# Performance work log

Hardware: AMD Instinct MI355X
Metric: run time of the kernel (lower is better)

The kernel has to match this reference:

```python
import jax, jax.numpy as jnp
import numpy as np

EPS = 1e-5
NUM_HEADS = 16

def layernorm(x, g, b):
    mu = jnp.mean(x, axis=-1, keepdims=True)
    var = jnp.mean(jnp.square(x - mu), axis=-1, keepdims=True)
    return (x - mu) * jax.lax.rsqrt(var + EPS) * g + b

def setup_inputs() -> dict:
    key = jax.random.key(0)
    ks = jax.random.split(key, 5)
    B, N, C = 2, 2048, 1024
    s_in = 1.0 / np.sqrt(C)
    return {
        "x": jax.random.normal(ks[0], (B, N, C), jnp.float32),
        "ln1_g": jnp.ones((C,), jnp.float32),
        "ln1_b": jnp.zeros((C,), jnp.float32),
        "w_qk": jax.random.normal(ks[1], (C, 2 * C), jnp.float32) * s_in,
        "w_v": jax.random.normal(ks[2], (C, C), jnp.float32) * s_in,
        "ln2_g": jnp.ones((C,), jnp.float32),
        "ln2_b": jnp.zeros((C,), jnp.float32),
        "w_proj": jax.random.normal(ks[3], (C, C), jnp.float32) * s_in,
        "b_proj": jnp.zeros((C,), jnp.float32),
    }

def reference(x, ln1_g, ln1_b, w_qk, w_v, ln2_g, ln2_b, w_proj, b_proj):
    B, N, C = x.shape
    H = NUM_HEADS
    hd = C // H
    scale = hd ** (-0.5)
    xn = layernorm(x, ln1_g, ln1_b)
    # qk: [B,N,2C] -> q,k each [B,H,N,hd]
    qk = (xn @ w_qk).reshape(B, N, 2, H, hd).transpose(2, 0, 3, 1, 4)
    q, k = qk[0], qk[1]
    v = (xn @ w_v).reshape(B, N, H, hd).transpose(0, 2, 1, 3)  # [B,H,N,hd]
    attn = jnp.einsum("bhqd,bhkd->bhqk", q, k) * scale
    attn = jax.nn.softmax(attn, axis=-1)
    out = jnp.einsum("bhqk,bhkd->bhqd", attn, v)  # [B,H,N,hd]
    out = out.transpose(0, 2, 1, 3).reshape(B, N, C)
    out = layernorm(out, ln2_g, ln2_b)
    return out @ w_proj + b_proj
```

## Files before the change

kernel.cpp:

```cpp
#include <hip/hip_runtime.h>
#include <hip/hip_bf16.h>


typedef __attribute__((ext_vector_type(8))) short short8;
typedef __attribute__((ext_vector_type(4))) short short4v;
typedef __attribute__((ext_vector_type(4))) float float4v;

__device__ __forceinline__ unsigned short f2bf(float f) {
    unsigned u = __builtin_bit_cast(unsigned, f);
    return (unsigned short)((u + 0x7FFFu + ((u >> 16) & 1u)) >> 16);
}
__device__ __forceinline__ unsigned packbf2(float lo, float hi) {
    return __builtin_amdgcn_perm(__builtin_bit_cast(unsigned, hi) + 0x8000u,
                                 __builtin_bit_cast(unsigned, lo) + 0x8000u,
                                 0x07060302u);
}
__device__ __forceinline__ void gll16(const unsigned short* g, unsigned short* l) {
    __builtin_amdgcn_global_load_lds(
        (const __attribute__((address_space(1))) unsigned int*)g,
        (__attribute__((address_space(3))) unsigned int*)l, 16, 0, 0);
}

__global__ __launch_bounds__(256) void prep(
    const float* __restrict__ x, const float* __restrict__ g1, const float* __restrict__ b1,
    const float* __restrict__ w_qk, const float* __restrict__ w_v,
    const float* __restrict__ w_proj, const float* __restrict__ g2,
    const float* __restrict__ b2,
    unsigned short* __restrict__ xn, unsigned short* __restrict__ wqkvT,
    unsigned short* __restrict__ wgT, float* __restrict__ u, float* __restrict__ w0) {
    __shared__ float sh[32 * 33];
    const int bid = blockIdx.x, tid = threadIdx.x;
    if (bid < 4096) {
        const float4 v = reinterpret_cast<const float4*>(x + (size_t)bid * 1024)[tid];
        float s  = v.x + v.y + v.z + v.w;
        float sq = v.x * v.x + v.y * v.y + v.z * v.z + v.w * v.w;
#pragma unroll
        for (int off = 32; off >= 1; off >>= 1) {
            s  += __shfl_xor(s, off, 64);
            sq += __shfl_xor(sq, off, 64);
        }
        const int w = tid >> 6, lane = tid & 63;
        if (lane == 0) { sh[w] = s; sh[4 + w] = sq; }
        __syncthreads();
        s  = sh[0] + sh[1] + sh[2] + sh[3];
        sq = sh[4] + sh[5] + sh[6] + sh[7];
        const float mu = s * (1.f / 1024.f);
        const float rstd = rsqrtf(sq * (1.f / 1024.f) - mu * mu + 1e-5f);
        const float4 gv = reinterpret_cast<const float4*>(g1)[tid];
        const float4 bv = reinterpret_cast<const float4*>(b1)[tid];
        ushort4 o;
        o.x = f2bf((v.x - mu) * rstd * gv.x + bv.x);
        o.y = f2bf((v.y - mu) * rstd * gv.y + bv.y);
        o.z = f2bf((v.z - mu) * rstd * gv.z + bv.z);
        o.w = f2bf((v.w - mu) * rstd * gv.w + bv.w);
        *reinterpret_cast<ushort4*>(&xn[(size_t)bid * 1024 + tid * 4]) = o;
    } else {
        const float* in; unsigned short* out; int Cc, bx, by; bool doU = false;
        if (bid < 6144)      { int t = bid - 4096; in = w_qk;   out = wqkvT;               Cc = 2048; bx = t & 63; by = t >> 6; }
        else if (bid < 7168) { int t = bid - 6144; in = w_v;    out = wqkvT + 2048 * 1024; Cc = 1024; bx = t & 31; by = t >> 5; }
        else                 { int t = bid - 7168; in = w_proj; out = wgT; doU = true;     Cc = 1024; bx = t & 31; by = t >> 5; }
        const int c0 = bx * 32, r0 = by * 32;
        const int tx = tid & 31, ty = tid >> 5;
#pragma unroll
        for (int i = 0; i < 32; i += 8)
            sh[(ty + i) * 33 + tx] = in[(size_t)(r0 + ty + i) * Cc + c0 + tx];
        __syncthreads();
        const float scale = doU ? g2[r0 + tx] : 1.f;
        const float b2v   = doU ? b2[r0 + tx] : 0.f;
#pragma unroll
        for (int i = 0; i < 32; i += 8) {
            const float raw = sh[tx * 33 + ty + i];
            const float sc  = raw * scale;
            out[(size_t)(c0 + ty + i) * 1024 + r0 + tx] = f2bf(sc);
            if (doU) {
                float pu = sc, pw = raw * b2v;
#pragma unroll
                for (int off = 1; off <= 16; off <<= 1) {
                    pu += __shfl_xor(pu, off, 64);
                    pw += __shfl_xor(pw, off, 64);
                }
                if (tx == 0) {
                    atomicAdd(&u[c0 + ty + i], pu);
                    atomicAdd(&w0[c0 + ty + i], pw);
                }
            }
        }
    }
}

__device__ __forceinline__ void stage_tiles(const unsigned short* __restrict__ A,
                                            const unsigned short* __restrict__ Bt,
                                            int K, int m0, int n0, int k0,
                                            unsigned short* As, unsigned short* Bs,
                                            int w, int ls, int sg) {
#pragma unroll
    for (int i = 0; i < 4; i++) {
        const int r = w * 32 + i * 8 + ls;
        const int g = (sg ^ ls) * 8;
        gll16(&A[(size_t)(m0 + r) * K + k0 + g], &As[(w * 32 + i * 8) * 64]);
        gll16(&Bt[(size_t)(n0 + r) * K + k0 + g], &Bs[(w * 32 + i * 8) * 64]);
    }
}

__device__ __forceinline__ void gemm128_core(const unsigned short* __restrict__ A,
                                             const unsigned short* __restrict__ Bt,
                                             int K, int m0, int n0,
                                             unsigned short* As, unsigned short* Bs,
                                             float4v acc[4][4]) {
    const int tid = threadIdx.x, lane = tid & 63, w = tid >> 6;
    const int wr = (w >> 1) * 64, wc = (w & 1) * 64;
    const int quad = lane >> 4, l16 = lane & 15;
    const int ls = lane >> 3, sg = lane & 7;
#pragma unroll
    for (int mi = 0; mi < 4; mi++)
#pragma unroll
        for (int ni = 0; ni < 4; ni++) acc[mi][ni] = float4v{0.f, 0.f, 0.f, 0.f};

    const int NS = K >> 6;
    stage_tiles(A, Bt, K, m0, n0, 0, As, Bs, w, ls, sg);
    for (int s = 0; s < NS; s++) {
        __syncthreads();
        const int cur = (s & 1) << 13;
        if (s + 1 < NS)
            stage_tiles(A, Bt, K, m0, n0, (s + 1) << 6,
                        As + (((s + 1) & 1) << 13), Bs + (((s + 1) & 1) << 13),
                        w, ls, sg);
        const unsigned short* Ac = As + cur;
        const unsigned short* Bc = Bs + cur;
#pragma unroll
        for (int ks = 0; ks < 2; ks++) {
            short8 af[4], bfr[4];
#pragma unroll
            for (int mi = 0; mi < 4; mi++) {
                const int r = wr + mi * 16 + l16;
                af[mi] = *reinterpret_cast<const short8*>(
                    &Ac[r * 64 + ((ks * 4 + quad) ^ (r & 7)) * 8]);
            }
#pragma unroll
            for (int ni = 0; ni < 4; ni++) {
                const int r = wc + ni * 16 + l16;
                bfr[ni] = *reinterpret_cast<const short8*>(
                    &Bc[r * 64 + ((ks * 4 + quad) ^ (r & 7)) * 8]);
            }
#pragma unroll
            for (int mi = 0; mi < 4; mi++)
#pragma unroll
                for (int ni = 0; ni < 4; ni++)
                    acc[mi][ni] = __builtin_amdgcn_mfma_f32_16x16x32_bf16(
                        af[mi], bfr[ni], acc[mi][ni], 0, 0, 0);
        }
    }
}

__global__ __launch_bounds__(256) void gemm128_qkv(const unsigned short* __restrict__ A,
                                                   const unsigned short* __restrict__ Bt,
                                                   unsigned short* __restrict__ qb,
                                                   unsigned short* __restrict__ kb,
                                                   unsigned short* __restrict__ vT) {
    __shared__ unsigned short As[2 * 128 * 64], Bs[2 * 128 * 64];
    const int m0 = blockIdx.y * 128, n0 = blockIdx.x * 128;
    float4v acc[4][4];
    gemm128_core(A, Bt, 1024, m0, n0, As, Bs, acc);
    const int lane = threadIdx.x & 63, w = threadIdx.x >> 6;
    const int wr = (w >> 1) * 64, wc = (w & 1) * 64;
    const int quad = lane >> 4, l16 = lane & 15;
    const float QSCALE = 0.125f * 1.4426950408889634f;
#pragma unroll
    for (int mi = 0; mi < 4; mi++) {
        const int row0 = m0 + wr + mi * 16 + quad * 4;
        const int b = row0 >> 11, nq = row0 & 2047;
#pragma unroll
        for (int ni = 0; ni < 4; ni++) {
            const int col = n0 + wc + ni * 16 + l16;
            if (col < 1024) {
                const int h = col >> 6, d = col & 63;
#pragma unroll
                for (int r = 0; r < 4; r++)
                    qb[(((size_t)b * 16 + h) * 2048 + nq + r) * 64 + d] =
                        f2bf(acc[mi][ni][r] * QSCALE);
            } else if (col < 2048) {
                const int c = col - 1024, h = c >> 6, d = c & 63;
#pragma unroll
                for (int r = 0; r < 4; r++)
                    kb[(((size_t)b * 16 + h) * 2048 + nq + r) * 64 + d] = f2bf(acc[mi][ni][r]);
            } else {
                const int c = col - 2048, h = c >> 6, d = c & 63;
                const short4v sv = {(short)f2bf(acc[mi][ni][0]), (short)f2bf(acc[mi][ni][1]),
                                    (short)f2bf(acc[mi][ni][2]), (short)f2bf(acc[mi][ni][3])};
                *reinterpret_cast<short4v*>(
                    &vT[(((size_t)b * 16 + h) * 64 + d) * 2048 + nq]) = sv;
            }
        }
    }
}

__global__ __launch_bounds__(256) void flash_attn(const unsigned short* __restrict__ qbuf,
                                                  const unsigned short* __restrict__ kb,
                                                  const unsigned short* __restrict__ vT,
                                                  unsigned short* __restrict__ attn,
                                                  float2* __restrict__ part) {
    __shared__ unsigned short Ks[64 * 64];
    __shared__ unsigned short Vs[64 * 64];
    const int tid = threadIdx.x, lane = tid & 63, w = tid >> 6;
    const int quad = lane >> 4, l16 = lane & 15;
    const int ls = lane >> 3, sg = lane & 7;
    const int qt = blockIdx.x, bh = blockIdx.y;
    const int q0 = qt * 128;
    const size_t nbase = (size_t)bh * 2048;

    short8 bq[2][2];
#pragma unroll
    for (int q2 = 0; q2 < 2; q2++)
#pragma unroll
        for (int ks = 0; ks < 2; ks++)
            bq[q2][ks] = *reinterpret_cast<const short8*>(
                &qbuf[(nbase + q0 + w * 32 + q2 * 16 + l16) * 64 + ks * 32 + quad * 8]);

    float l_part[2] = {0.f, 0.f};
    float4v o_acc[2][4];
#pragma unroll
    for (int q2 = 0; q2 < 2; q2++)
#pragma unroll
        for (int db = 0; db < 4; db++) o_acc[q2][db] = float4v{0.f, 0.f, 0.f, 0.f};

    for (int kt0 = 0; kt0 < 2048; kt0 += 64) {
        __syncthreads();
#pragma unroll
        for (int i = 0; i < 2; i++)
            gll16(&kb[(nbase + kt0 + w * 16 + i * 8 + ls) * 64 + ((sg ^ ls) << 3)],
                  &Ks[(w * 16 + i * 8) * 64]);
#pragma unroll
        for (int p = 0; p < 2; p++) {
            const int idx2 = p * 256 + tid;
            const int d = idx2 >> 3, G0 = (idx2 & 7) * 2;
            const uint4 vv = *reinterpret_cast<const uint4*>(
                &vT[((size_t)bh * 64 + d) * 2048 + kt0 + (G0 << 2)]);
            *reinterpret_cast<short4v*>(&Vs[(d << 6) + ((G0 ^ (d & 15)) << 2)]) =
                __builtin_bit_cast(short4v, uint2{vv.x, vv.y});
            *reinterpret_cast<short4v*>(&Vs[(d << 6) + (((G0 + 1) ^ (d & 15)) << 2)]) =
                __builtin_bit_cast(short4v, uint2{vv.z, vv.w});
        }
        __syncthreads();

        short8 kf[2][4];
#pragma unroll
        for (int ks = 0; ks < 2; ks++)
#pragma unroll
            for (int cb = 0; cb < 4; cb++) {
                const int r = cb * 16 + l16;
                kf[ks][cb] = *reinterpret_cast<const short8*>(
                    &Ks[r * 64 + ((ks * 4 + quad) ^ (r & 7)) * 8]);
            }
        short4v vb[4][4];
#pragma unroll
        for (int kt = 0; kt < 4; kt++)
#pragma unroll
            for (int db = 0; db < 4; db++)
                vb[kt][db] = *reinterpret_cast<const short4v*>(
                    &Vs[((db * 16 + l16) << 6) + (((kt * 4 + quad) ^ l16) << 2)]);

#pragma unroll
        for (int q2 = 0; q2 < 2; q2++) {
            float4v s_acc[4];
#pragma unroll
            for (int cb = 0; cb < 4; cb++) s_acc[cb] = float4v{0.f, 0.f, 0.f, 0.f};
#pragma unroll
            for (int ks = 0; ks < 2; ks++)
#pragma unroll
                for (int cb = 0; cb < 4; cb++)
                    s_acc[cb] = __builtin_amdgcn_mfma_f32_16x16x32_bf16(
                        kf[ks][cb], bq[q2][ks], s_acc[cb], 0, 0, 0);

            short4v pa[4];
            float ls2 = 0.f;
#pragma unroll
            for (int cb = 0; cb < 4; cb++) {
                const float p0 = __builtin_amdgcn_exp2f(s_acc[cb][0]);
                const float p1 = __builtin_amdgcn_exp2f(s_acc[cb][1]);
                const float p2 = __builtin_amdgcn_exp2f(s_acc[cb][2]);
                const float p3 = __builtin_amdgcn_exp2f(s_acc[cb][3]);
                ls2 += (p0 + p1) + (p2 + p3);
                pa[cb] = __builtin_bit_cast(short4v,
                          uint2{packbf2(p0, p1), packbf2(p2, p3)});
            }
            l_part[q2] += ls2;
#pragma unroll
            for (int kt = 0; kt < 4; kt++)
#pragma unroll
                for (int db = 0; db < 4; db++)
                    o_acc[q2][db] = __builtin_amdgcn_mfma_f32_16x16x16bf16_1k(
                        pa[kt], vb[kt][db], o_acc[q2][db], 0, 0, 0);
        }
    }

    const int b = bh >> 4, h = bh & 15;
#pragma unroll
    for (int q2 = 0; q2 < 2; q2++) {
        float lr = l_part[q2];
        lr += __shfl_xor(lr, 16, 64);
        lr += __shfl_xor(lr, 32, 64);
#pragma unroll
        for (int r = 0; r < 4; r++) {
            const float lq = __shfl(lr, quad * 4 + r, 64);
            const float inv = 1.f / lq;
            const int rowl = q0 + w * 32 + q2 * 16 + quad * 4 + r;
            const int grow = b * 2048 + rowl;
            float s = 0.f, s2 = 0.f;
#pragma unroll
            for (int db = 0; db < 4; db++) {
                const float on = o_acc[q2][db][r] * inv;
                attn[(size_t)grow * 1024 + h * 64 + db * 16 + l16] = f2bf(on);
                s += on;
                s2 = fmaf(on, on, s2);
            }
#pragma unroll
            for (int off = 1; off <= 8; off <<= 1) {
                s  += __shfl_xor(s, off, 64);
                s2 += __shfl_xor(s2, off, 64);
            }
            if (l16 == 0) part[(size_t)grow * 16 + h] = float2{s, s2};
        }
    }
}

__global__ __launch_bounds__(256) void gemm128_proj(const unsigned short* __restrict__ A,
                                                    const unsigned short* __restrict__ Bt,
                                                    const float2* __restrict__ part,
                                                    const float* __restrict__ u,
                                                    const float* __restrict__ w0,
                                                    const float* __restrict__ bias,
                                                    float* __restrict__ out) {
    __shared__ unsigned short As[2 * 128 * 64], Bs[2 * 128 * 64];
    __shared__ float2 rstat_s[128];
    const int m0 = blockIdx.y * 128, n0 = blockIdx.x * 128;
    {
        const int t = threadIdx.x, rloc = t >> 1, half = t & 1;
        const float4* p4 = reinterpret_cast<const float4*>(part);
        float s = 0.f, s2 = 0.f;
#pragma unroll
        for (int j = 0; j < 4; j++) {
            const float4 p = p4[(size_t)(m0 + rloc) * 8 + half * 4 + j];
            s += p.x + p.z; s2 += p.y + p.w;
        }
        s  += __shfl_xor(s, 1, 64);
        s2 += __shfl_xor(s2, 1, 64);
        if (!half) {
            const float mu = s * (1.f / 1024.f);
            const float rstd = rsqrtf(s2 * (1.f / 1024.f) - mu * mu + 1e-5f);
            rstat_s[rloc] = float2{rstd, mu * rstd};
        }
    }
    float4v acc[4][4];
    gemm128_core(A, Bt, 1024, m0, n0, As, Bs, acc);
    const int lane = threadIdx.x & 63, w = threadIdx.x >> 6;
    const int wr = (w >> 1) * 64, wc = (w & 1) * 64;
    const int quad = lane >> 4, l16 = lane & 15;
#pragma unroll
    for (int mi = 0; mi < 4; mi++) {
        const int rl0 = wr + mi * 16 + quad * 4;
        float2 rs[4];
#pragma unroll
        for (int r = 0; r < 4; r++) rs[r] = rstat_s[rl0 + r];
#pragma unroll
        for (int ni = 0; ni < 4; ni++) {
            const int col = n0 + wc + ni * 16 + l16;
            const float uu = u[col], ww = w0[col] + bias[col];
#pragma unroll
            for (int r = 0; r < 4; r++)
                out[(size_t)(m0 + rl0 + r) * 1024 + col] =
                    fmaf(rs[r].x, acc[mi][ni][r], ww - rs[r].y * uu);
        }
    }
}

extern "C" void kernel_launch(void* const* d_in, const int* in_sizes, int n_in,
                              void* d_out, int out_size, void* d_ws, size_t ws_size,
                              hipStream_t stream) {
    const float* x      = (const float*)d_in[0];
    const float* ln1_g  = (const float*)d_in[1];
    const float* ln1_b  = (const float*)d_in[2];
    const float* w_qk   = (const float*)d_in[3];
    const float* w_v    = (const float*)d_in[4];
    const float* ln2_g  = (const float*)d_in[5];
    const float* ln2_b  = (const float*)d_in[6];
    const float* w_proj = (const float*)d_in[7];
    const float* b_proj = (const float*)d_in[8];
    float* out = (float*)d_out;

    char* ws = (char*)d_ws;
    unsigned short* xn      = (unsigned short*)(ws + 0);
    unsigned short* wqkvT   = (unsigned short*)(ws + 8388608);
    unsigned short* wgT     = (unsigned short*)(ws + 14680064);
    unsigned short* qbuf    = (unsigned short*)(ws + 16777216);
    unsigned short* kbuf    = (unsigned short*)(ws + 25165824);
    unsigned short* vTbuf   = (unsigned short*)(ws + 33554432);
    unsigned short* attn    = (unsigned short*)(ws + 41943040);
    float2*         part    = (float2*)(ws + 50331648);
    float*          u       = (float*)(ws + 50888704);
    float*          w0      = (float*)(ws + 50892800);

    hipMemsetAsync(ws + 50888704, 0, 8192, stream);
    prep<<<8192, 256, 0, stream>>>(x, ln1_g, ln1_b, w_qk, w_v, w_proj, ln2_g, ln2_b,
                                   xn, wqkvT, wgT, u, w0);
    gemm128_qkv<<<dim3(24, 32), 256, 0, stream>>>(xn, wqkvT, qbuf, kbuf, vTbuf);
    flash_attn<<<dim3(16, 32), 256, 0, stream>>>(qbuf, kbuf, vTbuf, attn, part);
    gemm128_proj<<<dim3(8, 32), 256, 0, stream>>>(attn, wgT, part, u, w0, b_proj, out);
}
```

Measured before the change: 211.1 us.

## Use 256x256 QKV GEMM tiles and double-buffered 512-thread flash attention

Replaces the 128x128 QKV GEMM with a 256x256-tile, 512-thread kernel that keeps its own double-buffered K loop, raising operand reuse per block. Flash attention moves to 512 threads covering 256 queries per block and double-buffers the K/V tiles, so each iteration needs one barrier instead of two and loads overlap compute. The trade-off is fewer blocks (192 and 256), which leaves fewer waves in flight on a large-CU device, plus higher register and LDS pressure from the bigger accumulators.

```diff
diff --git a/kernel.cpp b/kernel.cpp
--- a/kernel.cpp
+++ b/kernel.cpp
@@ -88,6 +88,225 @@
     }
 }
 
+__global__ __launch_bounds__(512) void gemm256_qkv(const unsigned short* __restrict__ A,
+                                                   const unsigned short* __restrict__ Bt,
+                                                   unsigned short* __restrict__ qb,
+                                                   unsigned short* __restrict__ kb,
+                                                   unsigned short* __restrict__ vT) {
+    __shared__ unsigned short As[2 * 256 * 64], Bs[2 * 256 * 64];
+    const int tid = threadIdx.x, lane = tid & 63, w = tid >> 6;
+    const int wm = (w >> 2) * 128, wn = (w & 3) * 64;
+    const int quad = lane >> 4, l16 = lane & 15;
+    const int ls = lane >> 3, sg = lane & 7;
+    const int m0 = blockIdx.y * 256, n0 = blockIdx.x * 256;
+
+    float4v acc[8][4];
+#pragma unroll
+    for (int mi = 0; mi < 8; mi++)
+#pragma unroll
+        for (int ni = 0; ni < 4; ni++) acc[mi][ni] = float4v{0.f, 0.f, 0.f, 0.f};
+
+    const int g = (sg ^ ls) * 8;
+#pragma unroll 1
+    for (int s = -1; s < 16; s++) {
+        if (s >= 0) __syncthreads();
+        if (s + 1 < 16) {
+            const int k0 = (s + 1) << 6, buf = ((s + 1) & 1) << 14;
+            unsigned short* Ad = As + buf;
+            unsigned short* Bd = Bs + buf;
+#pragma unroll
+            for (int i = 0; i < 4; i++) {
+                const int r = w * 32 + i * 8 + ls;
+                gll16(&A[(size_t)(m0 + r) * 1024 + k0 + g], &Ad[(w * 32 + i * 8) * 64]);
+                gll16(&Bt[(size_t)(n0 + r) * 1024 + k0 + g], &Bd[(w * 32 + i * 8) * 64]);
+            }
+        }
+        if (s < 0) continue;
+        const unsigned short* Ac = As + ((s & 1) << 14);
+        const unsigned short* Bc = Bs + ((s & 1) << 14);
+#pragma unroll
+        for (int ks = 0; ks < 2; ks++) {
+            short8 af[8], bfr[4];
+#pragma unroll
+            for (int mi = 0; mi < 8; mi++) {
+                const int r = wm + mi * 16 + l16;
+                af[mi] = *reinterpret_cast<const short8*>(
+                    &Ac[r * 64 + ((ks * 4 + quad) ^ (r & 7)) * 8]);
+            }
+#pragma unroll
+            for (int ni = 0; ni < 4; ni++) {
+                const int r = wn + ni * 16 + l16;
+                bfr[ni] = *reinterpret_cast<const short8*>(
+                    &Bc[r * 64 + ((ks * 4 + quad) ^ (r & 7)) * 8]);
+            }
+#pragma unroll
+            for (int mi = 0; mi < 8; mi++)
+#pragma unroll
+                for (int ni = 0; ni < 4; ni++)
+                    acc[mi][ni] = __builtin_amdgcn_mfma_f32_16x16x32_bf16(
+                        af[mi], bfr[ni], acc[mi][ni], 0, 0, 0);
+        }
+    }
+
+    const float QSCALE = 0.125f * 1.4426950408889634f;
+#pragma unroll
+    for (int mi = 0; mi < 8; mi++) {
+        const int row0 = m0 + wm + mi * 16 + quad * 4;
+        const int b = row0 >> 11, nq = row0 & 2047;
+#pragma unroll
+        for (int ni = 0; ni < 4; ni++) {
+            const int col = n0 + wn + ni * 16 + l16;
+            if (col < 1024) {
+                const int h = col >> 6, d = col & 63;
+#pragma unroll
+                for (int r = 0; r < 4; r++)
+                    qb[(((size_t)b * 16 + h) * 2048 + nq + r) * 64 + d] =
+                        f2bf(acc[mi][ni][r] * QSCALE);
+            } else if (col < 2048) {
+                const int c = col - 1024, h = c >> 6, d = c & 63;
+#pragma unroll
+                for (int r = 0; r < 4; r++)
+                    kb[(((size_t)b * 16 + h) * 2048 + nq + r) * 64 + d] = f2bf(acc[mi][ni][r]);
+            } else {
+                const int c = col - 2048, h = c >> 6, d = c & 63;
+                const short4v sv = {(short)f2bf(acc[mi][ni][0]), (short)f2bf(acc[mi][ni][1]),
+                                    (short)f2bf(acc[mi][ni][2]), (short)f2bf(acc[mi][ni][3])};
+                *reinterpret_cast<short4v*>(
+                    &vT[(((size_t)b * 16 + h) * 64 + d) * 2048 + nq]) = sv;
+            }
+        }
+    }
+}
+
+__global__ __launch_bounds__(512) void flash_attn(const unsigned short* __restrict__ qbuf,
+                                                  const unsigned short* __restrict__ kb,
+                                                  const unsigned short* __restrict__ vT,
+                                                  unsigned short* __restrict__ attn,
+                                                  float2* __restrict__ part) {
+    __shared__ unsigned short Ks[2][64 * 64];
+    __shared__ unsigned short Vs[2][64 * 64];
+    const int tid = threadIdx.x, lane = tid & 63, w = tid >> 6;
+    const int quad = lane >> 4, l16 = lane & 15;
+    const int ls = lane >> 3, sg = lane & 7;
+    const int qt = blockIdx.x, bh = blockIdx.y;
+    const int q0 = qt * 256;
+    const size_t nbase = (size_t)bh * 2048;
+
+    short8 bq[2][2];
+#pragma unroll
+    for (int q2 = 0; q2 < 2; q2++)
+#pragma unroll
+        for (int ks = 0; ks < 2; ks++)
+            bq[q2][ks] = *reinterpret_cast<const short8*>(
+                &qbuf[(nbase + q0 + w * 32 + q2 * 16 + l16) * 64 + ks * 32 + quad * 8]);
+
+    float l_part[2] = {0.f, 0.f};
+    float4v o_acc[2][4];
+#pragma unroll
+    for (int q2 = 0; q2 < 2; q2++)
+#pragma unroll
+        for (int db = 0; db < 4; db++) o_acc[q2][db] = float4v{0.f, 0.f, 0.f, 0.f};
+
+    const int vd = tid >> 3, vG0 = (tid & 7) * 2;
+#pragma unroll 1
+    for (int s = -1; s < 32; s++) {
+        if (s >= 0) __syncthreads();
+        if (s + 1 < 32) {
+            const int kt0 = (s + 1) << 6, buf = (s + 1) & 1;
+            gll16(&kb[(nbase + kt0 + w * 8 + ls) * 64 + ((sg ^ ls) << 3)],
+                  &Ks[buf][(w * 8) * 64]);
+            const uint4 vv = *reinterpret_cast<const uint4*>(
+                &vT[((size_t)bh * 64 + vd) * 2048 + kt0 + (vG0 << 2)]);
+            *reinterpret_cast<short4v*>(&Vs[buf][(vd << 6) + ((vG0 ^ (vd & 15)) << 2)]) =
+                __builtin_bit_cast(short4v, uint2{vv.x, vv.y});
+            *reinterpret_cast<short4v*>(&Vs[buf][(vd << 6) + (((vG0 + 1) ^ (vd & 15)) << 2)]) =
+                __builtin_bit_cast(short4v, uint2{vv.z, vv.w});
+        }
+        if (s < 0) continue;
+        const unsigned short* Kc = Ks[s & 1];
+        const unsigned short* Vc = Vs[s & 1];
+
+        short8 kf[2][4];
+#pragma unroll
+        for (int ks = 0; ks < 2; ks++)
+#pragma unroll
+            for (int cb = 0; cb < 4; cb++) {
+                const int r = cb * 16 + l16;
+                kf[ks][cb] = *reinterpret_cast<const short8*>(
+                    &Kc[r * 64 + ((ks * 4 + quad) ^ (r & 7)) * 8]);
+            }
+        short4v vb[4][4];
+#pragma unroll
+        for (int kt = 0; kt < 4; kt++)
+#pragma unroll
+            for (int db = 0; db < 4; db++)
+                vb[kt][db] = *reinterpret_cast<const short4v*>(
+                    &Vc[((db * 16 + l16) << 6) + (((kt * 4 + quad) ^ l16) << 2)]);
+
+#pragma unroll
+        for (int q2 = 0; q2 < 2; q2++) {
+            float4v s_acc[4];
+#pragma unroll
+            for (int cb = 0; cb < 4; cb++) s_acc[cb] = float4v{0.f, 0.f, 0.f, 0.f};
+#pragma unroll
+            for (int ks = 0; ks < 2; ks++)
+#pragma unroll
+                for (int cb = 0; cb < 4; cb++)
+                    s_acc[cb] = __builtin_amdgcn_mfma_f32_16x16x32_bf16(
+                        kf[ks][cb], bq[q2][ks], s_acc[cb], 0, 0, 0);
+
+            short4v pa[4];
+            float ls2 = 0.f;
+#pragma unroll
+            for (int cb = 0; cb < 4; cb++) {
+                const float p0 = __builtin_amdgcn_exp2f(s_acc[cb][0]);
+                const float p1 = __builtin_amdgcn_exp2f(s_acc[cb][1]);
+                const float p2 = __builtin_amdgcn_exp2f(s_acc[cb][2]);
+                const float p3 = __builtin_amdgcn_exp2f(s_acc[cb][3]);
+                ls2 += (p0 + p1) + (p2 + p3);
+                pa[cb] = __builtin_bit_cast(short4v,
+                          uint2{packbf2(p0, p1), packbf2(p2, p3)});
+            }
+            l_part[q2] += ls2;
+#pragma unroll
+            for (int kt = 0; kt < 4; kt++)
+#pragma unroll
+                for (int db = 0; db < 4; db++)
+                    o_acc[q2][db] = __builtin_amdgcn_mfma_f32_16x16x16bf16_1k(
+                        pa[kt], vb[kt][db], o_acc[q2][db], 0, 0, 0);
+        }
+    }
+
+    const int b = bh >> 4, h = bh & 15;
+#pragma unroll
+    for (int q2 = 0; q2 < 2; q2++) {
+        float lr = l_part[q2];
+        lr += __shfl_xor(lr, 16, 64);
+        lr += __shfl_xor(lr, 32, 64);
+#pragma unroll
+        for (int r = 0; r < 4; r++) {
+            const float lq = __shfl(lr, quad * 4 + r, 64);
+            const float inv = 1.f / lq;
+            const int rowl = q0 + w * 32 + q2 * 16 + quad * 4 + r;
+            const int grow = b * 2048 + rowl;
+            float s = 0.f, s2 = 0.f;
+#pragma unroll
+            for (int db = 0; db < 4; db++) {
+                const float on = o_acc[q2][db][r] * inv;
+                attn[(size_t)grow * 1024 + h * 64 + db * 16 + l16] = f2bf(on);
+                s += on;
+                s2 = fmaf(on, on, s2);
+            }
+#pragma unroll
+            for (int off = 1; off <= 8; off <<= 1) {
+                s  += __shfl_xor(s, off, 64);
+                s2 += __shfl_xor(s2, off, 64);
+            }
+            if (l16 == 0) part[(size_t)grow * 16 + h] = float2{s, s2};
+        }
+    }
+}
+
 __device__ __forceinline__ void stage_tiles(const unsigned short* __restrict__ A,
                                             const unsigned short* __restrict__ Bt,
                                             int K, int m0, int n0, int k0,
@@ -148,177 +367,6 @@
                 for (int ni = 0; ni < 4; ni++)
                     acc[mi][ni] = __builtin_amdgcn_mfma_f32_16x16x32_bf16(
                         af[mi], bfr[ni], acc[mi][ni], 0, 0, 0);
-        }
-    }
-}
-
-__global__ __launch_bounds__(256) void gemm128_qkv(const unsigned short* __restrict__ A,
-                                                   const unsigned short* __restrict__ Bt,
-                                                   unsigned short* __restrict__ qb,
-                                                   unsigned short* __restrict__ kb,
-                                                   unsigned short* __restrict__ vT) {
-    __shared__ unsigned short As[2 * 128 * 64], Bs[2 * 128 * 64];
-    const int m0 = blockIdx.y * 128, n0 = blockIdx.x * 128;
-    float4v acc[4][4];
-    gemm128_core(A, Bt, 1024, m0, n0, As, Bs, acc);
-    const int lane = threadIdx.x & 63, w = threadIdx.x >> 6;
-    const int wr = (w >> 1) * 64, wc = (w & 1) * 64;
-    const int quad = lane >> 4, l16 = lane & 15;
-    const float QSCALE = 0.125f * 1.4426950408889634f;
-#pragma unroll
-    for (int mi = 0; mi < 4; mi++) {
-        const int row0 = m0 + wr + mi * 16 + quad * 4;
-        const int b = row0 >> 11, nq = row0 & 2047;
-#pragma unroll
-        for (int ni = 0; ni < 4; ni++) {
-            const int col = n0 + wc + ni * 16 + l16;
-            if (col < 1024) {
-                const int h = col >> 6, d = col & 63;
-#pragma unroll
-                for (int r = 0; r < 4; r++)
-                    qb[(((size_t)b * 16 + h) * 2048 + nq + r) * 64 + d] =
-                        f2bf(acc[mi][ni][r] * QSCALE);
-            } else if (col < 2048) {
-                const int c = col - 1024, h = c >> 6, d = c & 63;
-#pragma unroll
-                for (int r = 0; r < 4; r++)
-                    kb[(((size_t)b * 16 + h) * 2048 + nq + r) * 64 + d] = f2bf(acc[mi][ni][r]);
-            } else {
-                const int c = col - 2048, h = c >> 6, d = c & 63;
-                const short4v sv = {(short)f2bf(acc[mi][ni][0]), (short)f2bf(acc[mi][ni][1]),
-                                    (short)f2bf(acc[mi][ni][2]), (short)f2bf(acc[mi][ni][3])};
-                *reinterpret_cast<short4v*>(
-                    &vT[(((size_t)b * 16 + h) * 64 + d) * 2048 + nq]) = sv;
-            }
-        }
-    }
-}
-
-__global__ __launch_bounds__(256) void flash_attn(const unsigned short* __restrict__ qbuf,
-                                                  const unsigned short* __restrict__ kb,
-                                                  const unsigned short* __restrict__ vT,
-                                                  unsigned short* __restrict__ attn,
-                                                  float2* __restrict__ part) {
-    __shared__ unsigned short Ks[64 * 64];
-    __shared__ unsigned short Vs[64 * 64];
-    const int tid = threadIdx.x, lane = tid & 63, w = tid >> 6;
-    const int quad = lane >> 4, l16 = lane & 15;
-    const int ls = lane >> 3, sg = lane & 7;
-    const int qt = blockIdx.x, bh = blockIdx.y;
-    const int q0 = qt * 128;
-    const size_t nbase = (size_t)bh * 2048;
-
-    short8 bq[2][2];
-#pragma unroll
-    for (int q2 = 0; q2 < 2; q2++)
-#pragma unroll
-        for (int ks = 0; ks < 2; ks++)
-            bq[q2][ks] = *reinterpret_cast<const short8*>(
-                &qbuf[(nbase + q0 + w * 32 + q2 * 16 + l16) * 64 + ks * 32 + quad * 8]);
-
-    float l_part[2] = {0.f, 0.f};
-    float4v o_acc[2][4];
-#pragma unroll
-    for (int q2 = 0; q2 < 2; q2++)
-#pragma unroll
-        for (int db = 0; db < 4; db++) o_acc[q2][db] = float4v{0.f, 0.f, 0.f, 0.f};
-
-    for (int kt0 = 0; kt0 < 2048; kt0 += 64) {
-        __syncthreads();
-#pragma unroll
-        for (int i = 0; i < 2; i++)
-            gll16(&kb[(nbase + kt0 + w * 16 + i * 8 + ls) * 64 + ((sg ^ ls) << 3)],
-                  &Ks[(w * 16 + i * 8) * 64]);
-#pragma unroll
-        for (int p = 0; p < 2; p++) {
-            const int idx2 = p * 256 + tid;
-            const int d = idx2 >> 3, G0 = (idx2 & 7) * 2;
-            const uint4 vv = *reinterpret_cast<const uint4*>(
-                &vT[((size_t)bh * 64 + d) * 2048 + kt0 + (G0 << 2)]);
-            *reinterpret_cast<short4v*>(&Vs[(d << 6) + ((G0 ^ (d & 15)) << 2)]) =
-                __builtin_bit_cast(short4v, uint2{vv.x, vv.y});
-            *reinterpret_cast<short4v*>(&Vs[(d << 6) + (((G0 + 1) ^ (d & 15)) << 2)]) =
-                __builtin_bit_cast(short4v, uint2{vv.z, vv.w});
-        }
-        __syncthreads();
-
-        short8 kf[2][4];
-#pragma unroll
-        for (int ks = 0; ks < 2; ks++)
-#pragma unroll
-            for (int cb = 0; cb < 4; cb++) {
-                const int r = cb * 16 + l16;
-                kf[ks][cb] = *reinterpret_cast<const short8*>(
-                    &Ks[r * 64 + ((ks * 4 + quad) ^ (r & 7)) * 8]);
-            }
-        short4v vb[4][4];
-#pragma unroll
-        for (int kt = 0; kt < 4; kt++)
-#pragma unroll
-            for (int db = 0; db < 4; db++)
-                vb[kt][db] = *reinterpret_cast<const short4v*>(
-                    &Vs[((db * 16 + l16) << 6) + (((kt * 4 + quad) ^ l16) << 2)]);
-
-#pragma unroll
-        for (int q2 = 0; q2 < 2; q2++) {
-            float4v s_acc[4];
-#pragma unroll
-            for (int cb = 0; cb < 4; cb++) s_acc[cb] = float4v{0.f, 0.f, 0.f, 0.f};
-#pragma unroll
-            for (int ks = 0; ks < 2; ks++)
-#pragma unroll
-                for (int cb = 0; cb < 4; cb++)
-                    s_acc[cb] = __builtin_amdgcn_mfma_f32_16x16x32_bf16(
-                        kf[ks][cb], bq[q2][ks], s_acc[cb], 0, 0, 0);
-
-            short4v pa[4];
-            float ls2 = 0.f;
-#pragma unroll
-            for (int cb = 0; cb < 4; cb++) {
-                const float p0 = __builtin_amdgcn_exp2f(s_acc[cb][0]);
-                const float p1 = __builtin_amdgcn_exp2f(s_acc[cb][1]);
-                const float p2 = __builtin_amdgcn_exp2f(s_acc[cb][2]);
-                const float p3 = __builtin_amdgcn_exp2f(s_acc[cb][3]);
-                ls2 += (p0 + p1) + (p2 + p3);
-                pa[cb] = __builtin_bit_cast(short4v,
-                          uint2{packbf2(p0, p1), packbf2(p2, p3)});
-            }
-            l_part[q2] += ls2;
-#pragma unroll
-            for (int kt = 0; kt < 4; kt++)
-#pragma unroll
-                for (int db = 0; db < 4; db++)
-                    o_acc[q2][db] = __builtin_amdgcn_mfma_f32_16x16x16bf16_1k(
-                        pa[kt], vb[kt][db], o_acc[q2][db], 0, 0, 0);
-        }
-    }
-
-    const int b = bh >> 4, h = bh & 15;
-#pragma unroll
-    for (int q2 = 0; q2 < 2; q2++) {
-        float lr = l_part[q2];
-        lr += __shfl_xor(lr, 16, 64);
-        lr += __shfl_xor(lr, 32, 64);
-#pragma unroll
-        for (int r = 0; r < 4; r++) {
-            const float lq = __shfl(lr, quad * 4 + r, 64);
-            const float inv = 1.f / lq;
-            const int rowl = q0 + w * 32 + q2 * 16 + quad * 4 + r;
-            const int grow = b * 2048 + rowl;
-            float s = 0.f, s2 = 0.f;
-#pragma unroll
-            for (int db = 0; db < 4; db++) {
-                const float on = o_acc[q2][db][r] * inv;
-                attn[(size_t)grow * 1024 + h * 64 + db * 16 + l16] = f2bf(on);
-                s += on;
-                s2 = fmaf(on, on, s2);
-            }
-#pragma unroll
-            for (int off = 1; off <= 8; off <<= 1) {
-                s  += __shfl_xor(s, off, 64);
-                s2 += __shfl_xor(s2, off, 64);
-            }
-            if (l16 == 0) part[(size_t)grow * 16 + h] = float2{s, s2};
         }
     }
 }
@@ -402,7 +450,7 @@
     hipMemsetAsync(ws + 50888704, 0, 8192, stream);
     prep<<<8192, 256, 0, stream>>>(x, ln1_g, ln1_b, w_qk, w_v, w_proj, ln2_g, ln2_b,
                                    xn, wqkvT, wgT, u, w0);
-    gemm128_qkv<<<dim3(24, 32), 256, 0, stream>>>(xn, wqkvT, qbuf, kbuf, vTbuf);
-    flash_attn<<<dim3(16, 32), 256, 0, stream>>>(qbuf, kbuf, vTbuf, attn, part);
+    gemm256_qkv<<<dim3(12, 16), 512, 0, stream>>>(xn, wqkvT, qbuf, kbuf, vTbuf);
+    flash_attn<<<dim3(8, 32), 512, 0, stream>>>(qbuf, kbuf, vTbuf, attn, part);
     gemm128_proj<<<dim3(8, 32), 256, 0, stream>>>(attn, wgT, part, u, w0, b_proj, out);
 }
```

New measurement: 221.1 us. 1.05x slower.
